# Performance work log

Hardware: AMD Instinct MI355X
Metric: run time of the kernel (lower is better)

The kernel has to match this reference:

```python
import jax, jax.numpy as jnp
import numpy as np

D_MODEL = 512
N_HEADS = 8
HEAD_DIM = D_MODEL // N_HEADS
B, T = 128, 256


def setup_inputs() -> dict:
    key = jax.random.key(0)
    ks = jax.random.split(key, 5)
    s = 1.0 / np.sqrt(D_MODEL)
    return {
        "x": jax.random.normal(ks[0], (B, T, D_MODEL), dtype=jnp.float32),
        "W_qkv": jax.random.uniform(ks[1], (D_MODEL, 3 * D_MODEL), jnp.float32, -s, s),
        "b_qkv": jax.random.uniform(ks[2], (3 * D_MODEL,), jnp.float32, -s, s),
        "W_out": jax.random.uniform(ks[3], (D_MODEL, D_MODEL), jnp.float32, -s, s),
        "b_out": jax.random.uniform(ks[4], (D_MODEL,), jnp.float32, -s, s),
    }


def reference(x, W_qkv, b_qkv, W_out, b_out):
    Bsz, Tlen, C = x.shape
    H, hd = N_HEADS, HEAD_DIM
    qkv = x @ W_qkv + b_qkv                       # [B,T,3C]
    qkv = qkv.reshape(Bsz, Tlen, 3, H, hd).transpose(2, 0, 3, 1, 4)  # [3,B,H,T,hd]
    q, k, v = qkv[0], qkv[1], qkv[2]
    att = jnp.einsum('bhtd,bhsd->bhts', q, k) * (1.0 / np.sqrt(hd))  # [B,H,T,T]
    causal = jnp.tril(jnp.ones((Tlen, Tlen), dtype=bool))
    att = jnp.where(causal, att, -jnp.inf)
    att = jax.nn.softmax(att, axis=-1)
    y = jnp.einsum('bhts,bhsd->bhtd', att, v)     # [B,H,T,hd]
    y = y.transpose(0, 2, 1, 3).reshape(Bsz, Tlen, C)
    return y @ W_out + b_out
```

## Files before the change

### kernel.cpp

```cpp
#include <hip/hip_runtime.h>
#include <hip/hip_bf16.h>

typedef __attribute__((ext_vector_type(4))) float f32x4;
typedef __attribute__((ext_vector_type(8))) short s16x8;
typedef unsigned short u16;

__device__ __forceinline__ u16 f2bf(float f) {
    union { float f; unsigned int u; } a; a.f = f;
    unsigned int u = a.u;
    unsigned int lsb = (u >> 16) & 1u;
    u += 0x7fffu + lsb;
    return (u16)(u >> 16);
}

__device__ __forceinline__ void gll16(const u16* g, u16* l) {
    __builtin_amdgcn_global_load_lds(
        (const __attribute__((address_space(1))) unsigned int*)g,
        (__attribute__((address_space(3))) unsigned int*)l, 16, 0, 0);
}


__global__ void cvt_x_kernel(const float* __restrict__ x, u16* __restrict__ xb, int n4) {
    int i = blockIdx.x * 256 + threadIdx.x;
    if (i < n4) {
        float4 v = ((const float4*)x)[i];
        ushort4 o;
        o.x = f2bf(v.x); o.y = f2bf(v.y); o.z = f2bf(v.z); o.w = f2bf(v.w);
        ((ushort4*)xb)[i] = o;
    }
}

template<int KK, int NN>
__global__ void cvt_wT_kernel(const float* __restrict__ w, u16* __restrict__ wt) {
    int id = blockIdx.x * 256 + threadIdx.x;
    if (id < NN * (KK / 8)) {
        int n = id % NN, kg = id / NN;
        union { u16 h[8]; int4 v; } o;
#pragma unroll
        for (int e = 0; e < 8; ++e) o.h[e] = f2bf(w[(kg * 8 + e) * NN + n]);
        *(int4*)&wt[n * KK + kg * 8] = o.v;
    }
}


template<int K>
__device__ __forceinline__ void gemm_tile(const u16* __restrict__ A, const u16* __restrict__ Bt,
                                          int m0, int n0, u16* As, u16* Bs, f32x4 (&acc)[4][4]) {
    const int tid  = threadIdx.x;
    const int lane = tid & 63, li = lane & 15, quad = lane >> 4;
    const int w = tid >> 6;
    const int wm = (w & 1) * 64, wn = (w >> 1) * 64;
    const int lr  = lane >> 3;
    const int lcA = (lane & 7) ^ lr;
    const int lt  = lane >> 5;

    for (int kt = 0; kt < K; kt += 64) {
#pragma unroll
        for (int j = 0; j < 4; ++j)
            gll16(&A[(m0 + w * 32 + j * 8 + lr) * K + kt + lcA * 8], &As[(w * 256 + j * 64) * 8]);
#pragma unroll
        for (int j = 0; j < 4; ++j) {
            int lcB = (lane & 7) ^ ((j * 2 + lt) & 7);
            gll16(&Bt[(n0 + w * 32 + j * 8 + lr) * K + kt + lcB * 8], &Bs[(w * 256 + j * 64) * 8]);
        }
        __syncthreads();
#pragma unroll
        for (int kc = 0; kc < 2; ++kc) {
            const int sw = ((quad + kc * 4) ^ (li & 7)) * 8;
            s16x8 af[4], bfr[4];
#pragma unroll
            for (int i = 0; i < 4; ++i)
                af[i] = *(const s16x8*)&As[(wm + i * 16 + li) * 64 + sw];
#pragma unroll
            for (int j = 0; j < 4; ++j)
                bfr[j] = *(const s16x8*)&Bs[(wn + li * 4 + j) * 64 + sw];
#pragma unroll
            for (int i = 0; i < 4; ++i)
#pragma unroll
                for (int j = 0; j < 4; ++j)
                    acc[i][j] = __builtin_amdgcn_mfma_f32_16x16x32_bf16(af[i], bfr[j], acc[i][j], 0, 0, 0);
        }
        __syncthreads();
    }
}


__global__ __launch_bounds__(256) void gemm_qkv_kernel(const u16* __restrict__ xb,
                                                       const u16* __restrict__ WqkvT,
                                                       const float* __restrict__ b_qkv,
                                                       u16* __restrict__ Qb, u16* __restrict__ Kb,
                                                       u16* __restrict__ Vtb) {
    __shared__ __align__(16) u16 As[128 * 64];
    __shared__ __align__(16) u16 Bs[128 * 64];
    f32x4 acc[4][4];
#pragma unroll
    for (int i = 0; i < 4; ++i)
#pragma unroll
        for (int j = 0; j < 4; ++j) acc[i][j] = {0.f, 0.f, 0.f, 0.f};

    const int id = blockIdx.x, xcd = id & 7, slot = id >> 3;
    const int mt = xcd * 32 + slot / 12, nt = slot - (slot / 12) * 12;
    const int m0 = mt * 128, n0 = nt * 128;
    gemm_tile<512>(xb, WqkvT, m0, n0, As, Bs, acc);

    const int tid = threadIdx.x, lane = tid & 63, li = lane & 15, quad = lane >> 4, wave = tid >> 6;
    const int wm = (wave & 1) * 64, wn = (wave >> 1) * 64;
    const int c0 = n0 + wn;
    const int which = c0 >> 9, hh = (c0 >> 6) & 7;
    float4 b4 = *(const float4*)&b_qkv[c0 + li * 4];

#pragma unroll
    for (int i = 0; i < 4; ++i)
#pragma unroll
        for (int r = 0; r < 4; ++r) {
            int row = m0 + wm + i * 16 + quad * 4 + r;
            int bb = row >> 8, tt = row & 255;
            int bh = (bb * 8 + hh) << 14;
            u16 v0 = f2bf(acc[i][0][r] + b4.x), v1 = f2bf(acc[i][1][r] + b4.y);
            u16 v2 = f2bf(acc[i][2][r] + b4.z), v3 = f2bf(acc[i][3][r] + b4.w);
            if (which == 0) {
                *(ushort4*)&Qb[bh + tt * 64 + li * 4] = (ushort4){v0, v1, v2, v3};
            } else if (which == 1) {
                *(ushort4*)&Kb[bh + tt * 64 + li * 4] = (ushort4){v0, v1, v2, v3};
            } else {
                int vb = bh + (tt >> 5) * 2048 + (tt & 31);
                Vtb[vb + (li * 4 + 0) * 32] = v0;
                Vtb[vb + (li * 4 + 1) * 32] = v1;
                Vtb[vb + (li * 4 + 2) * 32] = v2;
                Vtb[vb + (li * 4 + 3) * 32] = v3;
            }
        }
}


__global__ __launch_bounds__(256) void gemm_out_kernel(const u16* __restrict__ Yb,
                                                       const u16* __restrict__ WoutT,
                                                       const float* __restrict__ b_out,
                                                       float* __restrict__ out) {
    __shared__ __align__(16) u16 As[128 * 64];
    __shared__ __align__(16) u16 Bs[128 * 64];
    f32x4 acc[4][4];
#pragma unroll
    for (int i = 0; i < 4; ++i)
#pragma unroll
        for (int j = 0; j < 4; ++j) acc[i][j] = {0.f, 0.f, 0.f, 0.f};

    const int id = blockIdx.x, xcd = id & 7, slot = id >> 3;
    const int mt = xcd * 32 + (slot >> 2), nt = slot & 3;
    const int m0 = mt * 128, n0 = nt * 128;
    gemm_tile<512>(Yb, WoutT, m0, n0, As, Bs, acc);

    const int tid = threadIdx.x, lane = tid & 63, li = lane & 15, quad = lane >> 4, wave = tid >> 6;
    const int wm = (wave & 1) * 64, wn = (wave >> 1) * 64;
    const int c0 = n0 + wn;
    float4 b4 = *(const float4*)&b_out[c0 + li * 4];

#pragma unroll
    for (int i = 0; i < 4; ++i)
#pragma unroll
        for (int r = 0; r < 4; ++r) {
            int row = m0 + wm + i * 16 + quad * 4 + r;
            float4 o;
            o.x = acc[i][0][r] + b4.x; o.y = acc[i][1][r] + b4.y;
            o.z = acc[i][2][r] + b4.z; o.w = acc[i][3][r] + b4.w;
            *(float4*)&out[row * 512 + c0 + li * 4] = o;
        }
}


__global__ __launch_bounds__(256, 2) void attn_kernel(const u16* __restrict__ Qb,
                                                      const u16* __restrict__ Kb,
                                                      const u16* __restrict__ Vtb,
                                                      u16* __restrict__ Yb) {
    __shared__ __align__(16) u16 Ks[256 * 64];
    __shared__ __align__(16) u16 pl[4 * 2 * 16 * 40];

    const int tid = threadIdx.x, wave = tid >> 6, lane = tid & 63, li = lane & 15, quad = lane >> 4;
    const int bhid = blockIdx.x;
    const int b = bhid >> 3, h = bhid & 7;
    const int bh = bhid << 14;

    s16x8 qf0 = *(const s16x8*)&Qb[bh + (wave * 16 + li) * 64 + quad * 8];
    s16x8 qf1 = *(const s16x8*)&Qb[bh + (wave * 16 + li) * 64 + 32 + quad * 8];

    {
        const int lr = lane >> 3;
        const int sg = (lane & 7) ^ lr;
#pragma unroll
        for (int j = 0; j < 8; ++j) {
            int blk = wave * 8 + j;
            gll16(&Kb[bh + (blk * 8 + lr) * 64 + sg * 8], &Ks[blk * 512]);
        }
    }
    __syncthreads();

    u16* plw = &pl[wave * 1280];

    for (int p = 0; p < 4; ++p) {
        const int qt = p * 4 + wave;
        const int qrb = qt * 16;
        const int nst = qt + 1;

        f32x4 sacc[16];
#pragma unroll
        for (int st = 0; st < 16; ++st) sacc[st] = {0.f, 0.f, 0.f, 0.f};
        const int sw = li & 7;
#pragma unroll
        for (int g = 0; g < 4; ++g) {
            if (g * 4 < nst) {
                s16x8 kf[4][2];
#pragma unroll
                for (int t = 0; t < 4; ++t) {
                    if (g * 4 + t < nst) {
                        int rb = ((g * 4 + t) * 16 + li) * 64;
                        kf[t][0] = *(const s16x8*)&Ks[rb + ((quad    ) ^ sw) * 8];
                        kf[t][1] = *(const s16x8*)&Ks[rb + ((quad + 4) ^ sw) * 8];
                    }
                }
#pragma unroll
                for (int t = 0; t < 4; ++t) {
                    if (g * 4 + t < nst) {
                        sacc[g*4+t] = __builtin_amdgcn_mfma_f32_16x16x32_bf16(qf0, kf[t][0], sacc[g*4+t], 0, 0, 0);
                        sacc[g*4+t] = __builtin_amdgcn_mfma_f32_16x16x32_bf16(qf1, kf[t][1], sacc[g*4+t], 0, 0, 0);
                    }
                }
            }
        }

        s16x8 nqf0 = qf0, nqf1 = qf1;
        if (p < 3) {
            int nqrb = ((p + 1) * 4 + wave) * 16;
            nqf0 = *(const s16x8*)&Qb[bh + (nqrb + li) * 64 + quad * 8];
            nqf1 = *(const s16x8*)&Qb[bh + (nqrb + li) * 64 + 32 + quad * 8];
        }

        float mx[4] = {-3e38f, -3e38f, -3e38f, -3e38f};
#pragma unroll
        for (int st = 0; st < 16; ++st) {
            if (st < nst) {
                int sg2 = st * 16 + li;
#pragma unroll
                for (int r = 0; r < 4; ++r) {
                    int tg = qrb + quad * 4 + r;
                    float v = (sg2 <= tg) ? sacc[st][r] * 0.125f : -3e38f;
                    sacc[st][r] = v;
                    mx[r] = fmaxf(mx[r], v);
                }
            }
        }
#pragma unroll
        for (int d = 1; d < 16; d <<= 1)
#pragma unroll
            for (int r = 0; r < 4; ++r) mx[r] = fmaxf(mx[r], __shfl_xor(mx[r], d, 64));

        const int ns32 = (nst + 1) >> 1;
        float l[4] = {0.f, 0.f, 0.f, 0.f};
        f32x4 oacc[4];
#pragma unroll
        for (int dt = 0; dt < 4; ++dt) oacc[dt] = {0.f, 0.f, 0.f, 0.f};

        s16x8 vf[2][4];
#pragma unroll
        for (int dt = 0; dt < 4; ++dt)
            vf[0][dt] = *(const s16x8*)&Vtb[bh + (li * 4 + dt) * 32 + quad * 8];

#pragma unroll
        for (int c = 0; c < 8; ++c) {
            if (c < ns32) {
                if (c + 1 < ns32) {
#pragma unroll
                    for (int dt = 0; dt < 4; ++dt)
                        vf[(c + 1) & 1][dt] = *(const s16x8*)&Vtb[bh + (c + 1) * 2048 + (li * 4 + dt) * 32 + quad * 8];
                }
                u16* pb = plw + (c & 1) * 640;
#pragma unroll
                for (int half = 0; half < 2; ++half) {
                    int st = c * 2 + half;
#pragma unroll
                    for (int r = 0; r < 4; ++r) {
                        float e = (st < nst) ? __expf(sacc[st][r] - mx[r]) : 0.f;
                        l[r] += e;
                        pb[(quad * 4 + r) * 40 + half * 16 + li] = f2bf(e);
                    }
                }
                s16x8 pf = *(const s16x8*)&pb[li * 40 + quad * 8];
#pragma unroll
                for (int dt = 0; dt < 4; ++dt)
                    oacc[dt] = __builtin_amdgcn_mfma_f32_16x16x32_bf16(pf, vf[c & 1][dt], oacc[dt], 0, 0, 0);
            }
        }

#pragma unroll
        for (int d = 1; d < 16; d <<= 1)
#pragma unroll
            for (int r = 0; r < 4; ++r) l[r] += __shfl_xor(l[r], d, 64);

#pragma unroll
        for (int r = 0; r < 4; ++r) {
            int tg = qrb + quad * 4 + r;
            float inv = 1.0f / l[r];
            ushort4 o;
            o.x = f2bf(oacc[0][r] * inv); o.y = f2bf(oacc[1][r] * inv);
            o.z = f2bf(oacc[2][r] * inv); o.w = f2bf(oacc[3][r] * inv);
            *(ushort4*)&Yb[(b * 256 + tg) * 512 + h * 64 + li * 4] = o;
        }

        qf0 = nqf0; qf1 = nqf1;
    }
}


extern "C" void kernel_launch(void* const* d_in, const int* in_sizes, int n_in,
                              void* d_out, int out_size, void* d_ws, size_t ws_size,
                              hipStream_t stream) {
    const float* x     = (const float*)d_in[0];
    const float* W_qkv = (const float*)d_in[1];
    const float* b_qkv = (const float*)d_in[2];
    const float* W_out = (const float*)d_in[3];
    const float* b_out = (const float*)d_in[4];
    float* out = (float*)d_out;

    char* ws = (char*)d_ws;
    u16* Qb    = (u16*)(ws);
    u16* Kb    = (u16*)(ws + 33554432);
    u16* Vtb   = (u16*)(ws + 67108864);
    u16* WqkvT = (u16*)(ws + 100663296);
    u16* WoutT = (u16*)(ws + 102236160);
    u16* xb    = (u16*)(ws + 102760448);
    u16* Yb    = xb;
    if (ws_size < (size_t)136314880) return;

    cvt_x_kernel<<<16384, 256, 0, stream>>>(x, xb, 4194304);
    cvt_wT_kernel<512, 1536><<<384, 256, 0, stream>>>(W_qkv, WqkvT);
    cvt_wT_kernel<512, 512><<<128, 256, 0, stream>>>(W_out, WoutT);
    gemm_qkv_kernel<<<3072, 256, 0, stream>>>(xb, WqkvT, b_qkv, Qb, Kb, Vtb);
    attn_kernel<<<1024, 256, 0, stream>>>(Qb, Kb, Vtb, Yb);
    gemm_out_kernel<<<1024, 256, 0, stream>>>(Yb, WoutT, b_out, out);
}
```

Before: 310.2 us.

## Use 256x256 double-buffered GEMM tiles with 512-thread blocks for projections

Both projection GEMMs move from 128x128 tiles with 256 threads to 256x256 tiles with 8 waves, each wave computing 128x64. The global-to-LDS loads now go into two LDS buffers, so the next K-slice is prefetched while the current one feeds the MFMAs. The aim is more data reuse per byte loaded and hiding load latency behind compute. In exchange each block needs 128KB of LDS and more accumulator registers, and the grid shrinks to 768 and 256 blocks, which makes wave quantization on the out GEMM a concern.

```diff
diff --git a/kernel.cpp b/kernel.cpp
--- a/kernel.cpp
+++ b/kernel.cpp
@@ -44,76 +44,96 @@
 
 
 template<int K>
-__device__ __forceinline__ void gemm_tile(const u16* __restrict__ A, const u16* __restrict__ Bt,
-                                          int m0, int n0, u16* As, u16* Bs, f32x4 (&acc)[4][4]) {
-    const int tid  = threadIdx.x;
-    const int lane = tid & 63, li = lane & 15, quad = lane >> 4;
-    const int w = tid >> 6;
-    const int wm = (w & 1) * 64, wn = (w >> 1) * 64;
-    const int lr  = lane >> 3;
-    const int lcA = (lane & 7) ^ lr;
-    const int lt  = lane >> 5;
-
-    for (int kt = 0; kt < K; kt += 64) {
-#pragma unroll
-        for (int j = 0; j < 4; ++j)
-            gll16(&A[(m0 + w * 32 + j * 8 + lr) * K + kt + lcA * 8], &As[(w * 256 + j * 64) * 8]);
-#pragma unroll
-        for (int j = 0; j < 4; ++j) {
-            int lcB = (lane & 7) ^ ((j * 2 + lt) & 7);
-            gll16(&Bt[(n0 + w * 32 + j * 8 + lr) * K + kt + lcB * 8], &Bs[(w * 256 + j * 64) * 8]);
+__device__ __forceinline__ void stage256(const u16* __restrict__ A, const u16* __restrict__ Bt,
+                                         int m0, int n0, int kt, u16* As, u16* Bs) {
+    const int lane = threadIdx.x & 63, w = threadIdx.x >> 6;
+    const int lr = lane >> 3;
+    const int lg = lane & 7;
+    const int sgA = lg ^ lr;
+#pragma unroll
+    for (int j = 0; j < 4; ++j) {
+        const int blk = w * 4 + j;
+        gll16(&A[(m0 + blk * 8 + lr) * K + kt + sgA * 8], &As[blk * 512]);
+    }
+#pragma unroll
+    for (int j = 0; j < 4; ++j) {
+        const int blk = w * 4 + j;
+        const int sgB = lg ^ ((2 * j + (lr >> 2)) & 7);
+        gll16(&Bt[(n0 + blk * 8 + lr) * K + kt + sgB * 8], &Bs[blk * 512]);
+    }
+}
+
+template<int K>
+__device__ __forceinline__ void gemm_tile256(const u16* __restrict__ A, const u16* __restrict__ Bt,
+                                             int m0, int n0,
+                                             u16* As0, u16* Bs0, u16* As1, u16* Bs1,
+                                             f32x4 (&acc)[8][4]) {
+    const int lane = threadIdx.x & 63, li = lane & 15, quad = lane >> 4;
+    const int w = threadIdx.x >> 6;
+    const int wr = w >> 2, wc = w & 3;
+    const int sw = li & 7;
+
+    stage256<K>(A, Bt, m0, n0, 0, As0, Bs0);
+    __syncthreads();
+
+#pragma unroll
+    for (int kt = 0; kt < K / 64; ++kt) {
+        u16* Asc = (kt & 1) ? As1 : As0;
+        u16* Bsc = (kt & 1) ? Bs1 : Bs0;
+        if (kt + 1 < K / 64)
+            stage256<K>(A, Bt, m0, n0, (kt + 1) * 64,
+                        (kt & 1) ? As0 : As1, (kt & 1) ? Bs0 : Bs1);
+#pragma unroll
+        for (int kc = 0; kc < 2; ++kc) {
+            s16x8 af[8], bf[4];
+#pragma unroll
+            for (int i = 0; i < 8; ++i)
+                af[i] = *(const s16x8*)&Asc[(wr * 128 + i * 16 + li) * 64 + (((quad + kc * 4) ^ sw)) * 8];
+#pragma unroll
+            for (int j = 0; j < 4; ++j)
+                bf[j] = *(const s16x8*)&Bsc[(wc * 64 + li * 4 + j) * 64 + (((quad + kc * 4) ^ sw)) * 8];
+#pragma unroll
+            for (int i = 0; i < 8; ++i)
+#pragma unroll
+                for (int j = 0; j < 4; ++j)
+                    acc[i][j] = __builtin_amdgcn_mfma_f32_16x16x32_bf16(af[i], bf[j], acc[i][j], 0, 0, 0);
         }
         __syncthreads();
-#pragma unroll
-        for (int kc = 0; kc < 2; ++kc) {
-            const int sw = ((quad + kc * 4) ^ (li & 7)) * 8;
-            s16x8 af[4], bfr[4];
-#pragma unroll
-            for (int i = 0; i < 4; ++i)
-                af[i] = *(const s16x8*)&As[(wm + i * 16 + li) * 64 + sw];
-#pragma unroll
-            for (int j = 0; j < 4; ++j)
-                bfr[j] = *(const s16x8*)&Bs[(wn + li * 4 + j) * 64 + sw];
-#pragma unroll
-            for (int i = 0; i < 4; ++i)
-#pragma unroll
-                for (int j = 0; j < 4; ++j)
-                    acc[i][j] = __builtin_amdgcn_mfma_f32_16x16x32_bf16(af[i], bfr[j], acc[i][j], 0, 0, 0);
-        }
-        __syncthreads();
-    }
-}
-
-
-__global__ __launch_bounds__(256) void gemm_qkv_kernel(const u16* __restrict__ xb,
-                                                       const u16* __restrict__ WqkvT,
-                                                       const float* __restrict__ b_qkv,
-                                                       u16* __restrict__ Qb, u16* __restrict__ Kb,
-                                                       u16* __restrict__ Vtb) {
-    __shared__ __align__(16) u16 As[128 * 64];
-    __shared__ __align__(16) u16 Bs[128 * 64];
-    f32x4 acc[4][4];
-#pragma unroll
-    for (int i = 0; i < 4; ++i)
+    }
+}
+
+
+__global__ __launch_bounds__(512, 2) void gemm_qkv_kernel(const u16* __restrict__ xb,
+                                                          const u16* __restrict__ WqkvT,
+                                                          const float* __restrict__ b_qkv,
+                                                          u16* __restrict__ Qb, u16* __restrict__ Kb,
+                                                          u16* __restrict__ Vtb) {
+    __shared__ __align__(16) u16 As0[256 * 64];
+    __shared__ __align__(16) u16 Bs0[256 * 64];
+    __shared__ __align__(16) u16 As1[256 * 64];
+    __shared__ __align__(16) u16 Bs1[256 * 64];
+    f32x4 acc[8][4];
+#pragma unroll
+    for (int i = 0; i < 8; ++i)
 #pragma unroll
         for (int j = 0; j < 4; ++j) acc[i][j] = {0.f, 0.f, 0.f, 0.f};
 
     const int id = blockIdx.x, xcd = id & 7, slot = id >> 3;
-    const int mt = xcd * 32 + slot / 12, nt = slot - (slot / 12) * 12;
-    const int m0 = mt * 128, n0 = nt * 128;
-    gemm_tile<512>(xb, WqkvT, m0, n0, As, Bs, acc);
-
-    const int tid = threadIdx.x, lane = tid & 63, li = lane & 15, quad = lane >> 4, wave = tid >> 6;
-    const int wm = (wave & 1) * 64, wn = (wave >> 1) * 64;
-    const int c0 = n0 + wn;
+    const int mt = xcd * 16 + slot / 6, nt = slot % 6;
+    const int m0 = mt * 256, n0 = nt * 256;
+    gemm_tile256<512>(xb, WqkvT, m0, n0, As0, Bs0, As1, Bs1, acc);
+
+    const int lane = threadIdx.x & 63, li = lane & 15, quad = lane >> 4;
+    const int w = threadIdx.x >> 6, wr = w >> 2, wc = w & 3;
+    const int c0 = n0 + wc * 64;
     const int which = c0 >> 9, hh = (c0 >> 6) & 7;
     float4 b4 = *(const float4*)&b_qkv[c0 + li * 4];
 
 #pragma unroll
-    for (int i = 0; i < 4; ++i)
+    for (int i = 0; i < 8; ++i)
 #pragma unroll
         for (int r = 0; r < 4; ++r) {
-            int row = m0 + wm + i * 16 + quad * 4 + r;
+            int row = m0 + wr * 128 + i * 16 + quad * 4 + r;
             int bb = row >> 8, tt = row & 255;
             int bh = (bb * 8 + hh) << 14;
             u16 v0 = f2bf(acc[i][0][r] + b4.x), v1 = f2bf(acc[i][1][r] + b4.y);
@@ -133,33 +153,35 @@
 }
 
 
-__global__ __launch_bounds__(256) void gemm_out_kernel(const u16* __restrict__ Yb,
-                                                       const u16* __restrict__ WoutT,
-                                                       const float* __restrict__ b_out,
-                                                       float* __restrict__ out) {
-    __shared__ __align__(16) u16 As[128 * 64];
-    __shared__ __align__(16) u16 Bs[128 * 64];
-    f32x4 acc[4][4];
-#pragma unroll
-    for (int i = 0; i < 4; ++i)
+__global__ __launch_bounds__(512, 2) void gemm_out_kernel(const u16* __restrict__ Yb,
+                                                          const u16* __restrict__ WoutT,
+                                                          const float* __restrict__ b_out,
+                                                          float* __restrict__ out) {
+    __shared__ __align__(16) u16 As0[256 * 64];
+    __shared__ __align__(16) u16 Bs0[256 * 64];
+    __shared__ __align__(16) u16 As1[256 * 64];
+    __shared__ __align__(16) u16 Bs1[256 * 64];
+    f32x4 acc[8][4];
+#pragma unroll
+    for (int i = 0; i < 8; ++i)
 #pragma unroll
         for (int j = 0; j < 4; ++j) acc[i][j] = {0.f, 0.f, 0.f, 0.f};
 
     const int id = blockIdx.x, xcd = id & 7, slot = id >> 3;
-    const int mt = xcd * 32 + (slot >> 2), nt = slot & 3;
-    const int m0 = mt * 128, n0 = nt * 128;
-    gemm_tile<512>(Yb, WoutT, m0, n0, As, Bs, acc);
-
-    const int tid = threadIdx.x, lane = tid & 63, li = lane & 15, quad = lane >> 4, wave = tid >> 6;
-    const int wm = (wave & 1) * 64, wn = (wave >> 1) * 64;
-    const int c0 = n0 + wn;
+    const int mt = xcd * 16 + (slot >> 1), nt = slot & 1;
+    const int m0 = mt * 256, n0 = nt * 256;
+    gemm_tile256<512>(Yb, WoutT, m0, n0, As0, Bs0, As1, Bs1, acc);
+
+    const int lane = threadIdx.x & 63, li = lane & 15, quad = lane >> 4;
+    const int w = threadIdx.x >> 6, wr = w >> 2, wc = w & 3;
+    const int c0 = n0 + wc * 64;
     float4 b4 = *(const float4*)&b_out[c0 + li * 4];
 
 #pragma unroll
-    for (int i = 0; i < 4; ++i)
+    for (int i = 0; i < 8; ++i)
 #pragma unroll
         for (int r = 0; r < 4; ++r) {
-            int row = m0 + wm + i * 16 + quad * 4 + r;
+            int row = m0 + wr * 128 + i * 16 + quad * 4 + r;
             float4 o;
             o.x = acc[i][0][r] + b4.x; o.y = acc[i][1][r] + b4.y;
             o.z = acc[i][2][r] + b4.z; o.w = acc[i][3][r] + b4.w;
@@ -333,7 +355,7 @@
     cvt_x_kernel<<<16384, 256, 0, stream>>>(x, xb, 4194304);
     cvt_wT_kernel<512, 1536><<<384, 256, 0, stream>>>(W_qkv, WqkvT);
     cvt_wT_kernel<512, 512><<<128, 256, 0, stream>>>(W_out, WoutT);
-    gemm_qkv_kernel<<<3072, 256, 0, stream>>>(xb, WqkvT, b_qkv, Qb, Kb, Vtb);
+    gemm_qkv_kernel<<<768, 512, 0, stream>>>(xb, WqkvT, b_qkv, Qb, Kb, Vtb);
     attn_kernel<<<1024, 256, 0, stream>>>(Qb, Kb, Vtb, Yb);
-    gemm_out_kernel<<<1024, 256, 0, stream>>>(Yb, WoutT, b_out, out);
-}
+    gemm_out_kernel<<<256, 512, 0, stream>>>(Yb, WoutT, b_out, out);
+}
```

Measured after the change: 308.6 us. No clear change (-0.5%).
